# Kernel optimization log

Measured on AMD Instinct MI355X. Metric: run time of the kernel, lower is better.

The kernel has to match this reference:

```python
import jax, jax.numpy as jnp
import numpy as np

B, L, D = 4, 512, 128

def setup_inputs() -> dict:
    key = jax.random.key(0)
    k1, k2, k3, k4 = jax.random.split(key, 4)
    s = 1.0 / np.sqrt(D)
    return {
        "inp": jax.random.normal(k1, (B, L, D), dtype=jnp.float32),
        "Wu": jax.random.normal(k2, (D, D), dtype=jnp.float32) * s,
        "Ww": jax.random.normal(k3, (D, D), dtype=jnp.float32) * s,
        "Wv": jax.random.normal(k4, (1, D), dtype=jnp.float32) * s,
    }

def reference(inp, Wu, Ww, Wv):
    # inp: (B,L,D); torch Linear weights are (out,in), so y = x @ W.T
    qu = inp @ Wu.T                      # (B,L,D), u(inp)
    kw = inp @ Ww.T                      # (B,L,D), w(inp)
    # qu.unsqueeze(1) -> broadcast over i; kw.unsqueeze(2) -> broadcast over j
    # h[b,i,j,:] = tanh(u(inp)[b,j] + w(inp)[b,i])   (dropout = identity in eval)
    h = jnp.tanh(qu[:, None, :, :] + kw[:, :, None, :])   # (B,L,L,D)
    score = jnp.einsum('bijd,d->bij', h, Wv[0])           # (B,L,L)
    attn = jax.nn.softmax(score, axis=2)                  # softmax over keys j
    out = jnp.einsum('bij,bjd->bid', attn, inp)           # bmm(attn, inp)
    return out, attn
```

## Files before the change

### kernel.cpp

```cpp
#include <hip/hip_runtime.h>

#define BD 128
#define SL 512
#define NB 4

__device__ __forceinline__ float rcp_fast(float x) { return __builtin_amdgcn_rcpf(x); }

__global__ __launch_bounds__(256) void k_tr(const float* __restrict__ Wu,
                                            const float* __restrict__ Ww,
                                            float* __restrict__ WuT,
                                            float* __restrict__ WwT) {
    int idx = blockIdx.x * 256 + threadIdx.x;
    int k = idx >> 7, o = idx & 127;
    WuT[idx] = Wu[o * BD + k];
    WwT[idx] = Ww[o * BD + k];
}

__global__ __launch_bounds__(256) void k_qk(const float* __restrict__ inp,
                                            const float* __restrict__ WuT,
                                            const float* __restrict__ WwT,
                                            float* __restrict__ Equ2,
                                            float* __restrict__ Ekw) {
    __shared__ float sx[2][BD];
    const int t = threadIdx.x, m = t >> 7, o = t & 127;
    const int r0 = blockIdx.x * 2;
    const int b  = r0 >> 9;
    const int l0 = r0 & (SL - 1);
    const int jp = l0 >> 1;

    sx[t >> 7][t & 127] = inp[(size_t)r0 * BD + t];
    __syncthreads();

    const float* WT = m ? WwT : WuT;
    float acc0 = 0.f, acc1 = 0.f;
    #pragma unroll 4
    for (int k = 0; k < BD; k += 4) {
        float w0 = WT[(k + 0) * BD + o];
        float w1 = WT[(k + 1) * BD + o];
        float w2 = WT[(k + 2) * BD + o];
        float w3 = WT[(k + 3) * BD + o];
        float4 x0 = *(const float4*)&sx[0][k];
        float4 x1 = *(const float4*)&sx[1][k];
        acc0 = fmaf(x0.x, w0, acc0); acc0 = fmaf(x0.y, w1, acc0);
        acc0 = fmaf(x0.z, w2, acc0); acc0 = fmaf(x0.w, w3, acc0);
        acc1 = fmaf(x1.x, w0, acc1); acc1 = fmaf(x1.y, w1, acc1);
        acc1 = fmaf(x1.z, w2, acc1); acc1 = fmaf(x1.w, w3, acc1);
    }

    if (m == 0) {
        size_t base = (((size_t)b * 32 + (o >> 2)) * 256 + jp) * 8 + (o & 3);
        Equ2[base]     = __expf(2.f * acc0);
        Equ2[base + 4] = __expf(2.f * acc1);
    } else {
        Ekw[(size_t)(r0 + 0) * BD + o] = __expf(2.f * acc0);
        Ekw[(size_t)(r0 + 1) * BD + o] = __expf(2.f * acc1);
    }
}

__global__ __launch_bounds__(1024, 8) void k_attn(const float* __restrict__ inp,
                                                  const float* __restrict__ Wv,
                                                  const float* __restrict__ Equ2,
                                                  const float* __restrict__ Ekw,
                                                  float* __restrict__ out,
                                                  float* __restrict__ attn) {
    __shared__ float4 smem4[(SL * 4 + 8960) / 4];
    float* smem  = (float*)smem4;
    float* s_pT  = smem;
    float* ovl   = smem + SL * 4;
    float4* s_E  = (float4*)ovl;
    float*  s_u  = ovl + 512;
    float*  s_ap = ovl;
    float*  s_rA = ovl + 8704;
    float*  s_rB = ovl + 8736;
    float*  s_fin= ovl;

    const int t  = threadIdx.x;
    const int b  = blockIdx.x >> 7;
    const int i0 = (blockIdx.x & 127) * 4;

    float4 eE; float eu;
    if (t < BD) {
        const float* ek = Ekw + ((size_t)b * SL + i0) * BD + t;
        float e0 = ek[0], e1 = ek[BD], e2 = ek[2 * BD], e3 = ek[3 * BD];
        eu = rcp_fast(Wv[t]);
        eE = make_float4(e0 * eu, e1 * eu, e2 * eu, e3 * eu);
    }
    if (t < BD) { s_E[t] = eE; s_u[t] = eu; }
    __syncthreads();

    const int jp = t & 255, dg = t >> 8;
    const float4* equ4 = (const float4*)(Equ2 + (size_t)b * BD * SL);
    float a0[4] = {0.f, 0.f, 0.f, 0.f};
    float a1[4] = {0.f, 0.f, 0.f, 0.f};
    #pragma unroll 2
    for (int cc = 0; cc < 8; ++cc) {
        int c = dg * 8 + cc;
        float4 qA = equ4[(c * 256 + jp) * 2 + 0];
        float4 qB = equ4[(c * 256 + jp) * 2 + 1];
        float qa[4] = {qA.x, qA.y, qA.z, qA.w};
        float qb[4] = {qB.x, qB.y, qB.z, qB.w};
        #pragma unroll
        for (int dd = 0; dd < 4; ++dd) {
            int d = c * 4 + dd;
            float4 E = s_E[d];
            float  u = s_u[d];
            a0[0] += rcp_fast(fmaf(qa[dd], E.x, u));
            a0[1] += rcp_fast(fmaf(qa[dd], E.y, u));
            a0[2] += rcp_fast(fmaf(qa[dd], E.z, u));
            a0[3] += rcp_fast(fmaf(qa[dd], E.w, u));
            a1[0] += rcp_fast(fmaf(qb[dd], E.x, u));
            a1[1] += rcp_fast(fmaf(qb[dd], E.y, u));
            a1[2] += rcp_fast(fmaf(qb[dd], E.z, u));
            a1[3] += rcp_fast(fmaf(qb[dd], E.w, u));
        }
    }
    __syncthreads();
    #pragma unroll
    for (int i = 0; i < 4; ++i) {
        s_ap[((dg * 2 + 0) * 4 + i) * 256 + jp] = a0[i];
        s_ap[((dg * 2 + 1) * 4 + i) * 256 + jp] = a1[i];
    }
    __syncthreads();

    const int j = t & 511, dh = t >> 9, ro = dh * 2;
    const int jpp = j >> 1, jj = j & 1, w8 = j >> 6;
    float af[2];
    #pragma unroll
    for (int ii = 0; ii < 2; ++ii) {
        int r = ro + ii;
        af[ii] = s_ap[((0 * 2 + jj) * 4 + r) * 256 + jpp]
               + s_ap[((1 * 2 + jj) * 4 + r) * 256 + jpp]
               + s_ap[((2 * 2 + jj) * 4 + r) * 256 + jpp]
               + s_ap[((3 * 2 + jj) * 4 + r) * 256 + jpp];
    }

    float mn[2] = { af[0], af[1] };
    #pragma unroll
    for (int off = 32; off > 0; off >>= 1) {
        mn[0] = fminf(mn[0], __shfl_xor(mn[0], off, 64));
        mn[1] = fminf(mn[1], __shfl_xor(mn[1], off, 64));
    }
    if ((j & 63) == 0) { s_rA[(ro + 0) * 8 + w8] = mn[0]; s_rA[(ro + 1) * 8 + w8] = mn[1]; }
    __syncthreads();
    #pragma unroll
    for (int ii = 0; ii < 2; ++ii) {
        float4 r0 = *(const float4*)&s_rA[(ro + ii) * 8];
        float4 r1 = *(const float4*)&s_rA[(ro + ii) * 8 + 4];
        mn[ii] = fminf(fminf(fminf(r0.x, r0.y), fminf(r0.z, r0.w)),
                       fminf(fminf(r1.x, r1.y), fminf(r1.z, r1.w)));
    }

    float p[2] = { __expf(-2.f * (af[0] - mn[0])), __expf(-2.f * (af[1] - mn[1])) };
    float sm[2] = { p[0], p[1] };
    #pragma unroll
    for (int off = 32; off > 0; off >>= 1) {
        sm[0] += __shfl_xor(sm[0], off, 64);
        sm[1] += __shfl_xor(sm[1], off, 64);
    }
    if ((j & 63) == 0) { s_rB[(ro + 0) * 8 + w8] = sm[0]; s_rB[(ro + 1) * 8 + w8] = sm[1]; }
    __syncthreads();
    float n[2];
    #pragma unroll
    for (int ii = 0; ii < 2; ++ii) {
        float4 r0 = *(const float4*)&s_rB[(ro + ii) * 8];
        float4 r1 = *(const float4*)&s_rB[(ro + ii) * 8 + 4];
        float rs = rcp_fast((r0.x + r0.y) + (r0.z + r0.w) + (r1.x + r1.y) + (r1.z + r1.w));
        n[ii] = p[ii] * rs;
        attn[((size_t)b * SL + i0 + ro + ii) * SL + j] = n[ii];
    }
    ((float2*)s_pT)[j * 2 + dh] = make_float2(n[0], n[1]);
    __syncthreads();

    const int g  = t >> 6;
    const int ln = t & 63;
    const int dq = ln & 31;
    const int rh = ln >> 5;
    const float4* inp4 = (const float4*)(inp + (size_t)b * SL * BD);
    float4 acc0 = make_float4(0.f, 0.f, 0.f, 0.f);
    float4 acc1 = make_float4(0.f, 0.f, 0.f, 0.f);
    #pragma unroll 4
    for (int jjj = 0; jjj < 32; ++jjj) {
        int jr = g * 32 + jjj;
        float4 x  = inp4[jr * 32 + dq];
        float2 pp = ((const float2*)s_pT)[jr * 2 + rh];
        acc0.x = fmaf(pp.x, x.x, acc0.x); acc0.y = fmaf(pp.x, x.y, acc0.y);
        acc0.z = fmaf(pp.x, x.z, acc0.z); acc0.w = fmaf(pp.x, x.w, acc0.w);
        acc1.x = fmaf(pp.y, x.x, acc1.x); acc1.y = fmaf(pp.y, x.y, acc1.y);
        acc1.z = fmaf(pp.y, x.z, acc1.z); acc1.w = fmaf(pp.y, x.w, acc1.w);
    }
    *(float4*)&s_fin[((g * 4) + rh * 2 + 0) * BD + dq * 4] = acc0;
    *(float4*)&s_fin[((g * 4) + rh * 2 + 1) * BD + dq * 4] = acc1;
    __syncthreads();
    if (t < 512) {
        int row = t >> 7, d = t & 127;
        float s = 0.f;
        #pragma unroll
        for (int gg = 0; gg < 16; ++gg)
            s += s_fin[(gg * 4 + row) * BD + d];
        out[((size_t)b * SL + i0 + row) * BD + d] = s;
    }
}

extern "C" void kernel_launch(void* const* d_in, const int* in_sizes, int n_in,
                              void* d_out, int out_size, void* d_ws, size_t ws_size,
                              hipStream_t stream) {
    const float* inp = (const float*)d_in[0];
    const float* Wu  = (const float*)d_in[1];
    const float* Ww  = (const float*)d_in[2];
    const float* Wv  = (const float*)d_in[3];

    float* out  = (float*)d_out;
    float* attn = out + (size_t)NB * SL * BD;

    float* ws   = (float*)d_ws;
    float* Equ2 = ws;
    float* Ekw  = Equ2 + (size_t)NB * BD * SL;
    float* WuT  = Ekw + (size_t)NB * SL * BD;
    float* WwT  = WuT + BD * BD;

    k_tr  <<<BD * BD / 256, 256, 0, stream>>>(Wu, Ww, WuT, WwT);
    k_qk  <<<NB * SL / 2, 256, 0, stream>>>(inp, WuT, WwT, Equ2, Ekw);
    k_attn<<<NB * SL / 4, 1024, 0, stream>>>(inp, Wv, Equ2, Ekw, out, attn);
}
```

Measured before the change: 94.94 us.

## Pair reciprocals via 1/a+1/b=(a+b)/ab, drop softmax max pass and sync

The inner attention loop now combines pairs of reciprocal terms as (a+b)*rcp(a*b), halving the number of transcendental rcp instructions in the dominant loop. The softmax min-reduction pass and its barrier are removed, relying on the score being bounded so exp(-2*af) cannot overflow. Shared memory is split into separate arrays, so s_ap no longer aliases s_E and the barrier before writing s_ap can be dropped. The trade-offs are possible precision loss or overflow in the product a*b, and a larger shared-memory footprint.

```diff
diff --git a/kernel.cpp b/kernel.cpp
--- a/kernel.cpp
+++ b/kernel.cpp
@@ -63,29 +63,22 @@
                                                   const float* __restrict__ Ekw,
                                                   float* __restrict__ out,
                                                   float* __restrict__ attn) {
-    __shared__ float4 smem4[(SL * 4 + 8960) / 4];
-    float* smem  = (float*)smem4;
-    float* s_pT  = smem;
-    float* ovl   = smem + SL * 4;
-    float4* s_E  = (float4*)ovl;
-    float*  s_u  = ovl + 512;
-    float*  s_ap = ovl;
-    float*  s_rA = ovl + 8704;
-    float*  s_rB = ovl + 8736;
-    float*  s_fin= ovl;
+    __shared__ float  s_pT[SL * 4];
+    __shared__ float  s_ap[8192];
+    __shared__ float4 s_E[BD];
+    __shared__ float  s_u[BD];
+    __shared__ float  s_rB[4 * 8];
 
     const int t  = threadIdx.x;
     const int b  = blockIdx.x >> 7;
     const int i0 = (blockIdx.x & 127) * 4;
 
-    float4 eE; float eu;
     if (t < BD) {
         const float* ek = Ekw + ((size_t)b * SL + i0) * BD + t;
-        float e0 = ek[0], e1 = ek[BD], e2 = ek[2 * BD], e3 = ek[3 * BD];
-        eu = rcp_fast(Wv[t]);
-        eE = make_float4(e0 * eu, e1 * eu, e2 * eu, e3 * eu);
-    }
-    if (t < BD) { s_E[t] = eE; s_u[t] = eu; }
+        float u = rcp_fast(Wv[t]);
+        s_E[t] = make_float4(ek[0] * u, ek[BD] * u, ek[2 * BD] * u, ek[3 * BD] * u);
+        s_u[t] = u;
+    }
     __syncthreads();
 
     const int jp = t & 255, dg = t >> 8;
@@ -97,24 +90,31 @@
         int c = dg * 8 + cc;
         float4 qA = equ4[(c * 256 + jp) * 2 + 0];
         float4 qB = equ4[(c * 256 + jp) * 2 + 1];
-        float qa[4] = {qA.x, qA.y, qA.z, qA.w};
-        float qb[4] = {qB.x, qB.y, qB.z, qB.w};
+        float4 E0 = s_E[c * 4 + 0];
+        float4 E1 = s_E[c * 4 + 1];
+        float4 E2 = s_E[c * 4 + 2];
+        float4 E3 = s_E[c * 4 + 3];
+        float4 uu = *(const float4*)&s_u[c * 4];
+        float e0[4] = {E0.x, E0.y, E0.z, E0.w};
+        float e1[4] = {E1.x, E1.y, E1.z, E1.w};
+        float e2[4] = {E2.x, E2.y, E2.z, E2.w};
+        float e3[4] = {E3.x, E3.y, E3.z, E3.w};
         #pragma unroll
-        for (int dd = 0; dd < 4; ++dd) {
-            int d = c * 4 + dd;
-            float4 E = s_E[d];
-            float  u = s_u[d];
-            a0[0] += rcp_fast(fmaf(qa[dd], E.x, u));
-            a0[1] += rcp_fast(fmaf(qa[dd], E.y, u));
-            a0[2] += rcp_fast(fmaf(qa[dd], E.z, u));
-            a0[3] += rcp_fast(fmaf(qa[dd], E.w, u));
-            a1[0] += rcp_fast(fmaf(qb[dd], E.x, u));
-            a1[1] += rcp_fast(fmaf(qb[dd], E.y, u));
-            a1[2] += rcp_fast(fmaf(qb[dd], E.z, u));
-            a1[3] += rcp_fast(fmaf(qb[dd], E.w, u));
+        for (int i = 0; i < 4; ++i) {
+            float xa0 = fmaf(qA.x, e0[i], uu.x);
+            float xa1 = fmaf(qA.y, e1[i], uu.y);
+            a0[i] = fmaf(xa0 + xa1, rcp_fast(xa0 * xa1), a0[i]);
+            float xa2 = fmaf(qA.z, e2[i], uu.z);
+            float xa3 = fmaf(qA.w, e3[i], uu.w);
+            a0[i] = fmaf(xa2 + xa3, rcp_fast(xa2 * xa3), a0[i]);
+            float xb0 = fmaf(qB.x, e0[i], uu.x);
+            float xb1 = fmaf(qB.y, e1[i], uu.y);
+            a1[i] = fmaf(xb0 + xb1, rcp_fast(xb0 * xb1), a1[i]);
+            float xb2 = fmaf(qB.z, e2[i], uu.z);
+            float xb3 = fmaf(qB.w, e3[i], uu.w);
+            a1[i] = fmaf(xb2 + xb3, rcp_fast(xb2 * xb3), a1[i]);
         }
     }
-    __syncthreads();
     #pragma unroll
     for (int i = 0; i < 4; ++i) {
         s_ap[((dg * 2 + 0) * 4 + i) * 256 + jp] = a0[i];
@@ -133,42 +133,28 @@
                + s_ap[((2 * 2 + jj) * 4 + r) * 256 + jpp]
                + s_ap[((3 * 2 + jj) * 4 + r) * 256 + jpp];
     }
-
-    float mn[2] = { af[0], af[1] };
+    float p0 = __expf(-2.f * af[0]);
+    float p1 = __expf(-2.f * af[1]);
+    float sm0 = p0, sm1 = p1;
     #pragma unroll
     for (int off = 32; off > 0; off >>= 1) {
-        mn[0] = fminf(mn[0], __shfl_xor(mn[0], off, 64));
-        mn[1] = fminf(mn[1], __shfl_xor(mn[1], off, 64));
-    }
-    if ((j & 63) == 0) { s_rA[(ro + 0) * 8 + w8] = mn[0]; s_rA[(ro + 1) * 8 + w8] = mn[1]; }
-    __syncthreads();
-    #pragma unroll
-    for (int ii = 0; ii < 2; ++ii) {
-        float4 r0 = *(const float4*)&s_rA[(ro + ii) * 8];
-        float4 r1 = *(const float4*)&s_rA[(ro + ii) * 8 + 4];
-        mn[ii] = fminf(fminf(fminf(r0.x, r0.y), fminf(r0.z, r0.w)),
-                       fminf(fminf(r1.x, r1.y), fminf(r1.z, r1.w)));
-    }
-
-    float p[2] = { __expf(-2.f * (af[0] - mn[0])), __expf(-2.f * (af[1] - mn[1])) };
-    float sm[2] = { p[0], p[1] };
-    #pragma unroll
-    for (int off = 32; off > 0; off >>= 1) {
-        sm[0] += __shfl_xor(sm[0], off, 64);
-        sm[1] += __shfl_xor(sm[1], off, 64);
-    }
-    if ((j & 63) == 0) { s_rB[(ro + 0) * 8 + w8] = sm[0]; s_rB[(ro + 1) * 8 + w8] = sm[1]; }
-    __syncthreads();
-    float n[2];
-    #pragma unroll
-    for (int ii = 0; ii < 2; ++ii) {
-        float4 r0 = *(const float4*)&s_rB[(ro + ii) * 8];
-        float4 r1 = *(const float4*)&s_rB[(ro + ii) * 8 + 4];
-        float rs = rcp_fast((r0.x + r0.y) + (r0.z + r0.w) + (r1.x + r1.y) + (r1.z + r1.w));
-        n[ii] = p[ii] * rs;
-        attn[((size_t)b * SL + i0 + ro + ii) * SL + j] = n[ii];
-    }
-    ((float2*)s_pT)[j * 2 + dh] = make_float2(n[0], n[1]);
+        sm0 += __shfl_xor(sm0, off, 64);
+        sm1 += __shfl_xor(sm1, off, 64);
+    }
+    if ((j & 63) == 0) { s_rB[(ro + 0) * 8 + w8] = sm0; s_rB[(ro + 1) * 8 + w8] = sm1; }
+    __syncthreads();
+    float n0, n1;
+    {
+        float4 r0 = *(const float4*)&s_rB[(ro + 0) * 8];
+        float4 r1 = *(const float4*)&s_rB[(ro + 0) * 8 + 4];
+        n0 = p0 * rcp_fast((r0.x + r0.y) + (r0.z + r0.w) + (r1.x + r1.y) + (r1.z + r1.w));
+        float4 s0 = *(const float4*)&s_rB[(ro + 1) * 8];
+        float4 s1 = *(const float4*)&s_rB[(ro + 1) * 8 + 4];
+        n1 = p1 * rcp_fast((s0.x + s0.y) + (s0.z + s0.w) + (s1.x + s1.y) + (s1.z + s1.w));
+    }
+    attn[((size_t)b * SL + i0 + ro + 0) * SL + j] = n0;
+    attn[((size_t)b * SL + i0 + ro + 1) * SL + j] = n1;
+    ((float2*)s_pT)[j * 2 + dh] = make_float2(n0, n1);
     __syncthreads();
 
     const int g  = t >> 6;
@@ -188,6 +174,7 @@
         acc1.x = fmaf(pp.y, x.x, acc1.x); acc1.y = fmaf(pp.y, x.y, acc1.y);
         acc1.z = fmaf(pp.y, x.z, acc1.z); acc1.w = fmaf(pp.y, x.w, acc1.w);
     }
+    float* s_fin = s_ap;
     *(float4*)&s_fin[((g * 4) + rh * 2 + 0) * BD + dq * 4] = acc0;
     *(float4*)&s_fin[((g * 4) + rh * 2 + 1) * BD + dq * 4] = acc1;
     __syncthreads();
```

New measurement: 89.69 us. 1.06x faster.
